# Kernel tuning notes

Hardware: AMD Instinct MI355X
Metric: run time of the kernel (lower is better)

The kernel has to match this reference:

```python
import jax, jax.numpy as jnp
import numpy as np

N, F, H, R, DEG, K = 8192, 64, 128, 3, 32, 32
TEMP = 0.3          # config.edge_temperature
NEG_SLOPE = 0.2     # LeakyReLU slope
EPS_LN = 1e-5
W_THRESH = 1e-6


def setup_inputs() -> dict:
    key = jax.random.key(0)
    ks = jax.random.split(key, 16)
    E = N * DEG
    # each node has DEG outgoing edges so no softmax row is empty (-inf everywhere)
    src = jnp.repeat(jnp.arange(N), DEG)
    tgt = jax.random.randint(ks[0], (E,), 0, N)
    edge_index = jnp.stack([src, tgt]).astype(jnp.int64)
    x = jax.random.normal(ks[1], (N, F), jnp.float32)
    edge_attr = jax.random.normal(ks[2], (E, 3), jnp.float32)
    s = lambda k, sh: jax.random.normal(k, sh, jnp.float32) * 0.05
    D = 2 * F + 3  # edge_input_dim
    params = dict(
        Ws1=s(ks[3], (D, H)), bs1=jnp.zeros(H), ln_g=jnp.ones(H), ln_b=jnp.zeros(H),
        Ws2=s(ks[4], (H, 1)), bs2=jnp.zeros(1),
        Wp=s(ks[5], (D, H)), bp=jnp.zeros(H),
        Wr1=s(ks[6], (F, H)), br1=jnp.zeros(H), Wr2=s(ks[7], (H, R)), br2=jnp.zeros(R),
        Wg1=s(ks[8], (R, H, H // 2)), bg1=jnp.zeros((R, H // 2)),
        Wg2=s(ks[9], (R, H // 2, 1)), bg2=jnp.zeros((R, 1)),
        Wc1=s(ks[10], (F, H)), bc1=jnp.zeros(H), Wc2=s(ks[11], (H, 1)), bc2=jnp.zeros(1),
    )
    return {"x": x, "edge_index": edge_index, "edge_attr": edge_attr, **params}


def reference(x, edge_index, edge_attr,
              Ws1, bs1, ln_g, ln_b, Ws2, bs2, Wp, bp,
              Wr1, br1, Wr2, br2, Wg1, bg1, Wg2, bg2,
              Wc1, bc1, Wc2, bc2):
    src, tgt = edge_index[0], edge_index[1]
    num_nodes = x.shape[0]

    # regime encoder on global mean state
    gs = x.mean(axis=0)
    regime_probs = jax.nn.softmax(jax.nn.relu(gs @ Wr1 + br1) @ Wr2 + br2)  # [R]

    # contagion detector (scalar level)
    contagion_level = jax.nn.sigmoid(jax.nn.relu(x @ Wc1 + bc1) @ Wc2 + bc2).mean()

    # gather -> edge MLP scorer with LayerNorm + LeakyReLU
    edge_input = jnp.concatenate([x[src], x[tgt], edge_attr], axis=-1)  # [E, 2F+3]
    h = edge_input @ Ws1 + bs1
    mu = h.mean(-1, keepdims=True)
    var = h.var(-1, keepdims=True)
    h = (h - mu) * jax.lax.rsqrt(var + EPS_LN) * ln_g + ln_b
    h = jnp.where(h >= 0, h, NEG_SLOPE * h)
    edge_scores_raw = h @ Ws2 + bs2  # [E, 1]

    # regime gating
    edge_hidden = jax.nn.relu(edge_input @ Wp + bp)  # [E, H]
    g1 = jax.nn.relu(jnp.einsum('eh,rhm->erm', edge_hidden, Wg1) + bg1)
    gates = jax.nn.sigmoid(jnp.einsum('erm,rmo->ero', g1, Wg2) + bg2)[..., 0]  # [E, R]
    gate_combined = (gates * regime_probs).sum(-1, keepdims=True)  # [E, 1]

    amp = 1.0 + 0.5 * contagion_level
    edge_scores = (edge_scores_raw * gate_combined * amp)[:, 0]  # [E]

    # scatter into dense NxN, masked softmax per source row, top-k
    M = jnp.full((num_nodes, num_nodes), -jnp.inf, x.dtype).at[src, tgt].set(edge_scores)
    P = jax.nn.softmax(M / TEMP, axis=-1)  # [N, N]
    topk_values, topk_indices = jax.lax.top_k(P, K)  # [N, K]

    # in-device compaction equivalent: weights below threshold zeroed (dropped edges)
    new_edge_weights = jnp.where(topk_values > W_THRESH, topk_values, 0.0)  # [N, K]
    return new_edge_weights, topk_indices
```

## Files before the change

kernel.cpp:

```cpp
#include <hip/hip_runtime.h>
#include <hip/hip_bf16.h>
#include <math.h>

#define NN 8192
#define FF 64
#define HH 128
#define RR 3
#define DEG 32
#define KK 32
#define EE (NN*DEG)
#define DD 131
#define TEMP 0.3f
#define NEG_SLOPE 0.2f
#define EPS_LN 1e-5f
#define W_THRESH 1e-6f

typedef float v2f __attribute__((ext_vector_type(2)));
__device__ __forceinline__ float4 ld4(const float* p) { return *(const float4*)p; }
#define PKFMA(a, b, c) __builtin_elementwise_fma((a), (b), (c))
#define AIDX(a, j) a[((j)>>2)*2 + (((j)&3)>>1)][(j)&1]
#define GIDX(r, g) gaccv[r][(g)>>1][(g)&1]


__global__ __launch_bounds__(256) void setup_kernel(
    const float* __restrict__ x,
    const float* __restrict__ Ws1, const float* __restrict__ Wp,
    const float* __restrict__ Wc1, const float* __restrict__ bc1,
    const float* __restrict__ Wc2, const float* __restrict__ bc2,
    float* __restrict__ PA, float* __restrict__ hdr)
{
    __shared__ float spool[12608];
    int t = threadIdx.x;
    int bid = blockIdx.x;

    if (bid < 512) {
        float* xs = spool;
        float* wl = spool + 2080;
        int which = bid & 1;
        int n0 = (bid >> 1) * 32;
        const float* base = which ? Wp : Ws1;

        for (int i = t; i < 2048; i += 256)
            xs[(i >> 6) * 65 + (i & 63)] = x[n0 * 64 + i];
        for (int it = 0; it < 8; it++) {
            int flat = (t + it * 256) * 4;
            *(float4*)&wl[flat] = ld4(&base[flat]);
        }
        __syncthreads();

        int row = t >> 3, colg = t & 7;
        float acc[16];
        #pragma unroll
        for (int j = 0; j < 16; j++) acc[j] = 0.f;
        const float* xr = &xs[row * 65];
        for (int k = 0; k < 64; k++) {
            float a = xr[k];
            const float* wr = &wl[k * 128 + colg * 16];
            #pragma unroll
            for (int jj = 0; jj < 4; jj++) {
                float4 w = ld4(wr + 4 * jj);
                acc[4*jj+0] += a * w.x; acc[4*jj+1] += a * w.y;
                acc[4*jj+2] += a * w.z; acc[4*jj+3] += a * w.w;
            }
        }
        float* outp = PA + (size_t)which * (NN * 128) + (size_t)(n0 + row) * 128 + colg * 16;
        #pragma unroll
        for (int j = 0; j < 16; j++) outp[j] = acc[j];
    } else {
        float* xs = spool;
        float* wl = spool + 4160;
        float* cs = spool + 12352;
        int n0 = (bid - 512) * 64;

        for (int i = 0; i < 16; i++) {
            int flat = t + i * 256;
            int r = flat >> 6, c = flat & 63;
            xs[r * 65 + c] = x[(n0 + r) * 64 + c];
        }
        for (int i = 0; i < 8; i++) {
            int flat = (t + i * 256) * 4;
            *(float4*)&wl[flat] = ld4(&Wc1[flat]);
        }
        __syncthreads();

        {
            int col = t & 63, g = t >> 6;
            float ps = 0.f;
            for (int r = g * 16; r < g * 16 + 16; r++) ps += xs[r * 65 + col];
            cs[g * 64 + col] = ps;
        }
        __syncthreads();
        if (t < 64) {
            float v = cs[t] + cs[64 + t] + cs[128 + t] + cs[192 + t];
            atomicAdd(&hdr[8 + t], v);
        }

        int r = t >> 2, q = t & 3;
        float accl = 0.f;
        for (int hh = 0; hh < 32; hh++) {
            int h = hh * 4 + q;
            float s = bc1[h];
            for (int i = 0; i < 64; i++) s += xs[r * 65 + i] * wl[i * 128 + h];
            accl += fmaxf(s, 0.f) * Wc2[h];
        }
        accl += __shfl_xor(accl, 1);
        accl += __shfl_xor(accl, 2);
        if (q == 0) {
            float lvl = 1.f / (1.f + expf(-(accl + bc2[0])));
            atomicAdd(&hdr[0], lvl);
        }
    }
}

__global__ __launch_bounds__(128) void regime_kernel(
    const float* __restrict__ Wr1, const float* __restrict__ br1,
    const float* __restrict__ Wr2, const float* __restrict__ br2,
    float* __restrict__ hdr)
{
    __shared__ float gsl[64];
    __shared__ float t1[128];
    int t = threadIdx.x;
    if (t < 64) gsl[t] = hdr[8 + t] * (1.f / (float)NN);
    __syncthreads();
    float a = br1[t];
    for (int i = 0; i < 64; i++) a += gsl[i] * Wr1[i * 128 + t];
    t1[t] = fmaxf(a, 0.f);
    __syncthreads();
    if (t < 3) {
        float v = br2[t];
        for (int h = 0; h < 128; h++) v += t1[h] * Wr2[h * 3 + t];
        gsl[32 + t] = v;
    }
    __syncthreads();
    if (t == 0) {
        float v0 = gsl[32], v1 = gsl[33], v2 = gsl[34];
        float m = fmaxf(v0, fmaxf(v1, v2));
        float e0 = expf(v0 - m), e1 = expf(v1 - m), e2 = expf(v2 - m);
        float inv = 1.f / (e0 + e1 + e2);
        hdr[1] = e0 * inv; hdr[2] = e1 * inv; hdr[3] = e2 * inv;
        hdr[4] = 1.f + 0.5f * (hdr[0] * (1.f / (float)NN));
    }
}

#define EIB_S 76
__global__ __launch_bounds__(256) void edge_fused_kernel(
    const int* __restrict__ tgt_idx, const float* __restrict__ edge_attr,
    const float* __restrict__ x,
    const float* __restrict__ Ws1, const float* __restrict__ bs1,
    const float* __restrict__ ln_g, const float* __restrict__ ln_b,
    const float* __restrict__ Ws2, const float* __restrict__ bs2,
    const float* __restrict__ Wp, const float* __restrict__ bp,
    const float* __restrict__ Wg1, const float* __restrict__ bg1,
    const float* __restrict__ Wg2, const float* __restrict__ bg2,
    const float* __restrict__ PA1, const float* __restrict__ PA2,
    const float* __restrict__ hdr, float* __restrict__ scores)
{
    __shared__ float pool[8000];
    float* EIB   = pool;
    float* WPan  = pool + 4864;
    float* ehTh  = pool;
    float* WgPan = pool + 4352;
    float* Gbuf  = pool;
    float* rawS  = pool + 7936;

    int t = threadIdx.x;
    int e0 = blockIdx.x * 64;

    {
        int r = t >> 2, q = t & 3;
        int ge = e0 + r;
        int tg = tgt_idx[ge];
        #pragma unroll
        for (int i = 0; i < 4; i++) {
            int col = q * 16 + 4 * i;
            *(float4*)&EIB[r * EIB_S + col] = ld4(&x[tg * 64 + col]);
        }
        if (q == 0) {
            float4 v;
            v.x = edge_attr[(size_t)ge * 3 + 0];
            v.y = edge_attr[(size_t)ge * 3 + 1];
            v.z = edge_attr[(size_t)ge * 3 + 2];
            v.w = 0.f;
            *(float4*)&EIB[r * EIB_S + 64] = v;
        } else if (q == 1) {
            *(float4*)&EIB[r * EIB_S + 68] = make_float4(0.f, 0.f, 0.f, 0.f);
        } else if (q == 2) {
            *(float4*)&EIB[r * EIB_S + 72] = make_float4(0.f, 0.f, 0.f, 0.f);
        }
    }

    int tcol = t & 7, trow = t >> 3;
    const float* EIr0 = &EIB[(2 * trow) * EIB_S];
    const float* EIr1 = EIr0 + EIB_S;
    int src = (e0 + 2 * trow) >> 5;

    v2f accs0[8], accs1[8], accp0[8], accp1[8];

    {
        const float* p1 = &PA1[(size_t)src * 128 + tcol * 4];
        const float* p2 = &PA2[(size_t)src * 128 + tcol * 4];
        #pragma unroll
        for (int jj = 0; jj < 4; jj++) {
            float4 v;
            v = ld4(p1 + jj * 32);
            v2f lo1 = { v.x, v.y }, hi1 = { v.z, v.w };
            accs0[jj*2] = lo1; accs0[jj*2+1] = hi1;
            accs1[jj*2] = lo1; accs1[jj*2+1] = hi1;
            v = ld4(p2 + jj * 32);
            v2f lo2 = { v.x, v.y }, hi2 = { v.z, v.w };
            accp0[jj*2] = lo2; accp0[jj*2+1] = hi2;
            accp1[jj*2] = lo2; accp1[jj*2+1] = hi2;
        }
    }

    for (int p = 0; p < 6; p++) {
        __syncthreads();
        #pragma unroll
        for (int i = 0; i < 3; i++) {
            int fid = i * 256 + t;
            int mat = (fid >= 384) ? 1 : 0;
            int loc = fid - mat * 384;
            int pr = loc >> 5;
            int pc = (loc & 31) * 4;
            int wrow = 64 + p * 12 + pr;
            const float* Wsrc = mat ? Wp : Ws1;
            float4 w = (wrow < 131) ? ld4(&Wsrc[wrow * 128 + pc])
                                    : make_float4(0.f, 0.f, 0.f, 0.f);
            *(float4*)&WPan[mat * 1536 + pr * 128 + pc] = w;
        }
        __syncthreads();
        for (int kk = 0; kk < 12; kk++) {
            int k = p * 12 + kk;
            float a0 = EIr0[k];
            float a1 = EIr1[k];
            v2f a0v = { a0, a0 }, a1v = { a1, a1 };
            const float* ws = &WPan[kk * 128 + tcol * 4];
            const float* wq = ws + 1536;
            #pragma unroll
            for (int jj = 0; jj < 4; jj++) {
                float4 w1 = ld4(ws + jj * 32);
                v2f w1a = { w1.x, w1.y }, w1b = { w1.z, w1.w };
                accs0[jj*2]   = PKFMA(a0v, w1a, accs0[jj*2]);
                accs0[jj*2+1] = PKFMA(a0v, w1b, accs0[jj*2+1]);
                accs1[jj*2]   = PKFMA(a1v, w1a, accs1[jj*2]);
                accs1[jj*2+1] = PKFMA(a1v, w1b, accs1[jj*2+1]);
                float4 w2 = ld4(wq + jj * 32);
                v2f w2a = { w2.x, w2.y }, w2b = { w2.z, w2.w };
                accp0[jj*2]   = PKFMA(a0v, w2a, accp0[jj*2]);
                accp0[jj*2+1] = PKFMA(a0v, w2b, accp0[jj*2+1]);
                accp1[jj*2]   = PKFMA(a1v, w2a, accp1[jj*2]);
                accp1[jj*2+1] = PKFMA(a1v, w2b, accp1[jj*2+1]);
            }
        }
    }

    {
        float s0 = 0.f, ss0 = 0.f, s1 = 0.f, ss1 = 0.f;
        #pragma unroll
        for (int j = 0; j < 16; j++) {
            int col = tcol * 4 + (j >> 2) * 32 + (j & 3);
            float b = bs1[col];
            float u0 = AIDX(accs0, j) + b;  AIDX(accs0, j) = u0;
            float u1 = AIDX(accs1, j) + b;  AIDX(accs1, j) = u1;
            s0 += u0; ss0 += u0 * u0;
            s1 += u1; ss1 += u1 * u1;
        }
        #pragma unroll
        for (int m = 1; m < 8; m <<= 1) {
            s0 += __shfl_xor(s0, m);  ss0 += __shfl_xor(ss0, m);
            s1 += __shfl_xor(s1, m);  ss1 += __shfl_xor(ss1, m);
        }
        float mu0 = s0 * (1.f / 128.f), mu1 = s1 * (1.f / 128.f);
        float var0 = ss0 * (1.f / 128.f) - mu0 * mu0;
        float var1 = ss1 * (1.f / 128.f) - mu1 * mu1;
        float inv0 = 1.f / sqrtf(var0 + EPS_LN);
        float inv1 = 1.f / sqrtf(var1 + EPS_LN);
        float d0 = 0.f, d1 = 0.f;
        #pragma unroll
        for (int j = 0; j < 16; j++) {
            int col = tcol * 4 + (j >> 2) * 32 + (j & 3);
            float g = ln_g[col], bb = ln_b[col], w2 = Ws2[col];
            float y0 = (AIDX(accs0, j) - mu0) * inv0 * g + bb;
            float y1 = (AIDX(accs1, j) - mu1) * inv1 * g + bb;
            y0 = (y0 >= 0.f) ? y0 : NEG_SLOPE * y0;
            y1 = (y1 >= 0.f) ? y1 : NEG_SLOPE * y1;
            d0 += y0 * w2; d1 += y1 * w2;
        }
        #pragma unroll
        for (int m = 1; m < 8; m <<= 1) {
            d0 += __shfl_xor(d0, m); d1 += __shfl_xor(d1, m);
        }
        if (tcol == 0) {
            rawS[2 * trow]     = d0 + bs2[0];
            rawS[2 * trow + 1] = d1 + bs2[0];
        }
    }

    int gtr = t >> 4, gtc = t & 15;
    int grow = t >> 2, gq = t & 3;

    v2f gaccv[3][8];
    #pragma unroll
    for (int rr = 0; rr < 3; rr++)
        #pragma unroll
        for (int j = 0; j < 8; j++) gaccv[rr][j] = (v2f){ 0.f, 0.f };

    for (int hf = 0; hf < 2; hf++) {
        __syncthreads();
        #pragma unroll
        for (int j2 = 0; j2 < 8; j2++) {
            int j = hf * 8 + j2;
            int col = tcol * 4 + (j >> 2) * 32 + (j & 3);
            int lc = col - hf * 64;
            float b = bp[col];
            ehTh[lc * 68 + 2 * trow]     = fmaxf(AIDX(accp0, j) + b, 0.f);
            ehTh[lc * 68 + 2 * trow + 1] = fmaxf(AIDX(accp1, j) + b, 0.f);
        }
        for (int p = 0; p < 4; p++) {
            __syncthreads();
            #pragma unroll
            for (int i = 0; i < 3; i++) {
                int fid = i * 256 + t;
                int rr = fid >> 8;
                int loc = fid & 255;
                int pr = loc >> 4;
                int pc = (loc & 15) * 4;
                *(float4*)&WgPan[rr * 1024 + pr * 64 + pc] =
                    ld4(&Wg1[(size_t)(rr * 128 + hf * 64 + p * 16 + pr) * 64 + pc]);
            }
            __syncthreads();
            for (int kk = 0; kk < 16; kk++) {
                float4 av = ld4(&ehTh[(p * 16 + kk) * 68 + 4 * gtr]);
                v2f ax = { av.x, av.x }, ay = { av.y, av.y };
                v2f az = { av.z, av.z }, aw = { av.w, av.w };
                #pragma unroll
                for (int rr = 0; rr < 3; rr++) {
                    float4 bv = ld4(&WgPan[rr * 1024 + kk * 64 + 4 * gtc]);
                    v2f bva = { bv.x, bv.y }, bvb = { bv.z, bv.w };
                    gaccv[rr][0] = PKFMA(ax, bva, gaccv[rr][0]);
                    gaccv[rr][1] = PKFMA(ax, bvb, gaccv[rr][1]);
                    gaccv[rr][2] = PKFMA(ay, bva, gaccv[rr][2]);
                    gaccv[rr][3] = PKFMA(ay, bvb, gaccv[rr][3]);
                    gaccv[rr][4] = PKFMA(az, bva, gaccv[rr][4]);
                    gaccv[rr][5] = PKFMA(az, bvb, gaccv[rr][5]);
                    gaccv[rr][6] = PKFMA(aw, bva, gaccv[rr][6]);
                    gaccv[rr][7] = PKFMA(aw, bvb, gaccv[rr][7]);
                }
            }
        }
    }

    float gc = 0.f;
    for (int rr = 0; rr < 3; rr++) {
        __syncthreads();
        #pragma unroll
        for (int j = 0; j < 4; j++) {
            float b = bg1[rr * 64 + 4 * gtc + j];
            float4 g;
            g.x = fmaxf(GIDX(rr, 0  + j) + b, 0.f);
            g.y = fmaxf(GIDX(rr, 4  + j) + b, 0.f);
            g.z = fmaxf(GIDX(rr, 8  + j) + b, 0.f);
            g.w = fmaxf(GIDX(rr, 12 + j) + b, 0.f);
            *(float4*)&Gbuf[(4 * gtc + j) * 68 + 4 * gtr] = g;
        }
        __syncthreads();
        float pacc = 0.f;
        #pragma unroll
        for (int j = 0; j < 16; j++) {
            int m = gq * 4 + (j >> 2) * 16 + (j & 3);
            pacc += Gbuf[m * 68 + grow] * Wg2[rr * 64 + m];
        }
        pacc += __shfl_xor(pacc, 1);
        pacc += __shfl_xor(pacc, 2);
        float gate = 1.f / (1.f + expf(-(pacc + bg2[rr])));
        gc += gate * hdr[1 + rr];
    }
    if (gq == 0) scores[e0 + grow] = rawS[grow] * gc * hdr[4];
}

__global__ __launch_bounds__(64) void finalize_kernel(
    const int* __restrict__ tgt_idx, const float* __restrict__ scores,
    float* __restrict__ out_w, float* __restrict__ out_i)
{
    __shared__ int   tl[32];
    __shared__ float pl[32];
    int j = threadIdx.x;
    int row = blockIdx.x;
    bool lane_active = (j < 32);
    int   tg = 0;
    float s  = -INFINITY;
    if (lane_active) {
        tg = tgt_idx[row * 32 + j];
        s  = scores[row * 32 + j];
        tl[j] = tg;
    }
    __syncthreads();

    bool alive = false;
    if (lane_active) {
        alive = true;
        for (int j2 = j + 1; j2 < 32; j2++)
            if (tl[j2] == tg) { alive = false; break; }
    }
    float z = (lane_active && alive) ? s * (1.f / TEMP) : -INFINITY;
    float m = z;
    #pragma unroll
    for (int mm = 1; mm < 64; mm <<= 1) m = fmaxf(m, __shfl_xor(m, mm));
    float p = (lane_active && alive) ? expf(z - m) : 0.f;
    float sum = p;
    #pragma unroll
    for (int mm = 1; mm < 64; mm <<= 1) sum += __shfl_xor(sum, mm);
    p = p / sum;
    if (lane_active) pl[j] = alive ? p : -1.f;
    __syncthreads();

    int rank = 0, dcount = 0;
    for (int j2 = 0; j2 < 32; j2++) {
        float pj = pl[j2];
        if (pj >= 0.f) {
            dcount++;
            if (lane_active && alive) {
                if (pj > p || (pj == p && tl[j2] < tg)) rank++;
            }
        }
    }
    if (lane_active && alive) {
        out_w[row * 32 + rank] = (p > W_THRESH) ? p : 0.f;
        out_i[row * 32 + rank] = (float)tg;
    }
    if (j == 0) {
        int c = 0;
        for (int slot = dcount; slot < 32; slot++) {
            for (;;) {
                bool found = false;
                for (int q = 0; q < 32; q++) if (tl[q] == c) { found = true; break; }
                if (!found) break;
                c++;
            }
            out_w[row * 32 + slot] = 0.f;
            out_i[row * 32 + slot] = (float)c;
            c++;
        }
    }
}

extern "C" void kernel_launch(void* const* d_in, const int* in_sizes, int n_in,
                              void* d_out, int out_size, void* d_ws, size_t ws_size,
                              hipStream_t stream)
{
    const float* x          = (const float*)d_in[0];
    const int*   edge_index = (const int*)  d_in[1];
    const float* edge_attr  = (const float*)d_in[2];
    const float* Ws1 = (const float*)d_in[3];
    const float* bs1 = (const float*)d_in[4];
    const float* ln_g = (const float*)d_in[5];
    const float* ln_b = (const float*)d_in[6];
    const float* Ws2 = (const float*)d_in[7];
    const float* bs2 = (const float*)d_in[8];
    const float* Wp  = (const float*)d_in[9];
    const float* bp  = (const float*)d_in[10];
    const float* Wr1 = (const float*)d_in[11];
    const float* br1 = (const float*)d_in[12];
    const float* Wr2 = (const float*)d_in[13];
    const float* br2 = (const float*)d_in[14];
    const float* Wg1 = (const float*)d_in[15];
    const float* bg1 = (const float*)d_in[16];
    const float* Wg2 = (const float*)d_in[17];
    const float* bg2 = (const float*)d_in[18];
    const float* Wc1 = (const float*)d_in[19];
    const float* bc1 = (const float*)d_in[20];
    const float* Wc2 = (const float*)d_in[21];
    const float* bc2 = (const float*)d_in[22];

    float* hdr    = (float*)d_ws;
    float* scores = hdr + 128;
    float* tabs   = scores + EE;
    const int* tgt = edge_index + EE;

    hipMemsetAsync(d_ws, 0, 512, stream);
    setup_kernel<<<640, 256, 0, stream>>>(x, Ws1, Wp, Wc1, bc1, Wc2, bc2, tabs, hdr);
    regime_kernel<<<1, 128, 0, stream>>>(Wr1, br1, Wr2, br2, hdr);
    edge_fused_kernel<<<EE / 64, 256, 0, stream>>>(
        tgt, edge_attr, x, Ws1, bs1, ln_g, ln_b, Ws2, bs2, Wp, bp,
        Wg1, bg1, Wg2, bg2, tabs, tabs + (size_t)NN * 128, hdr, scores);
    finalize_kernel<<<NN, 64, 0, stream>>>(
        tgt, scores, (float*)d_out, (float*)d_out + NN * KK);
}
```

Baseline: 444.6 us.

## Read edge-MLP and gate weights directly from global memory instead of LDS panels

Removes the LDS weight panels and their staging loops in the edge fused kernel, so Ws1/Wp and Wg1 rows are read straight from global memory (cached in L1/L2) inside the FMA loops. This eliminates many __syncthreads barriers and the panel copy traffic, and shrinks shared memory from 8000 to 4416 floats, allowing more resident blocks per CU. The cost is per-thread global loads in the inner loop, which may add latency that is harder to hide than LDS reads. The padding-column zeroing is dropped because the K loop now stops exactly at 67.

```diff
diff --git a/kernel.cpp b/kernel.cpp
--- a/kernel.cpp
+++ b/kernel.cpp
@@ -142,7 +142,7 @@
     }
 }
 
-#define EIB_S 76
+#define EIB_S 68
 __global__ __launch_bounds__(256) void edge_fused_kernel(
     const int* __restrict__ tgt_idx, const float* __restrict__ edge_attr,
     const float* __restrict__ x,
@@ -155,13 +155,11 @@
     const float* __restrict__ PA1, const float* __restrict__ PA2,
     const float* __restrict__ hdr, float* __restrict__ scores)
 {
-    __shared__ float pool[8000];
+    __shared__ float pool[4416];
     float* EIB   = pool;
-    float* WPan  = pool + 4864;
     float* ehTh  = pool;
-    float* WgPan = pool + 4352;
     float* Gbuf  = pool;
-    float* rawS  = pool + 7936;
+    float* rawS  = pool + 4352;
 
     int t = threadIdx.x;
     int e0 = blockIdx.x * 64;
@@ -182,10 +180,6 @@
             v.z = edge_attr[(size_t)ge * 3 + 2];
             v.w = 0.f;
             *(float4*)&EIB[r * EIB_S + 64] = v;
-        } else if (q == 1) {
-            *(float4*)&EIB[r * EIB_S + 68] = make_float4(0.f, 0.f, 0.f, 0.f);
-        } else if (q == 2) {
-            *(float4*)&EIB[r * EIB_S + 72] = make_float4(0.f, 0.f, 0.f, 0.f);
         }
     }
 
@@ -213,29 +207,18 @@
         }
     }
 
-    for (int p = 0; p < 6; p++) {
-        __syncthreads();
-        #pragma unroll
-        for (int i = 0; i < 3; i++) {
-            int fid = i * 256 + t;
-            int mat = (fid >= 384) ? 1 : 0;
-            int loc = fid - mat * 384;
-            int pr = loc >> 5;
-            int pc = (loc & 31) * 4;
-            int wrow = 64 + p * 12 + pr;
-            const float* Wsrc = mat ? Wp : Ws1;
-            float4 w = (wrow < 131) ? ld4(&Wsrc[wrow * 128 + pc])
-                                    : make_float4(0.f, 0.f, 0.f, 0.f);
-            *(float4*)&WPan[mat * 1536 + pr * 128 + pc] = w;
-        }
-        __syncthreads();
-        for (int kk = 0; kk < 12; kk++) {
-            int k = p * 12 + kk;
+    __syncthreads();
+
+    {
+        const float* wS = Ws1 + (size_t)64 * 128 + tcol * 4;
+        const float* wQ = Wp  + (size_t)64 * 128 + tcol * 4;
+        #pragma unroll 2
+        for (int k = 0; k < 64; k++) {
             float a0 = EIr0[k];
             float a1 = EIr1[k];
             v2f a0v = { a0, a0 }, a1v = { a1, a1 };
-            const float* ws = &WPan[kk * 128 + tcol * 4];
-            const float* wq = ws + 1536;
+            const float* ws = wS + (size_t)k * 128;
+            const float* wq = wQ + (size_t)k * 128;
             #pragma unroll
             for (int jj = 0; jj < 4; jj++) {
                 float4 w1 = ld4(ws + jj * 32);
@@ -252,6 +235,29 @@
                 accp1[jj*2+1] = PKFMA(a1v, w2b, accp1[jj*2+1]);
             }
         }
+        #pragma unroll
+        for (int i = 0; i < 3; i++) {
+            float a0 = EIr0[64 + i];
+            float a1 = EIr1[64 + i];
+            v2f a0v = { a0, a0 }, a1v = { a1, a1 };
+            const float* ws = Ws1 + (size_t)(128 + i) * 128 + tcol * 4;
+            const float* wq = Wp  + (size_t)(128 + i) * 128 + tcol * 4;
+            #pragma unroll
+            for (int jj = 0; jj < 4; jj++) {
+                float4 w1 = ld4(ws + jj * 32);
+                v2f w1a = { w1.x, w1.y }, w1b = { w1.z, w1.w };
+                accs0[jj*2]   = PKFMA(a0v, w1a, accs0[jj*2]);
+                accs0[jj*2+1] = PKFMA(a0v, w1b, accs0[jj*2+1]);
+                accs1[jj*2]   = PKFMA(a1v, w1a, accs1[jj*2]);
+                accs1[jj*2+1] = PKFMA(a1v, w1b, accs1[jj*2+1]);
+                float4 w2 = ld4(wq + jj * 32);
+                v2f w2a = { w2.x, w2.y }, w2b = { w2.z, w2.w };
+                accp0[jj*2]   = PKFMA(a0v, w2a, accp0[jj*2]);
+                accp0[jj*2+1] = PKFMA(a0v, w2b, accp0[jj*2+1]);
+                accp1[jj*2]   = PKFMA(a1v, w2a, accp1[jj*2]);
+                accp1[jj*2+1] = PKFMA(a1v, w2b, accp1[jj*2+1]);
+            }
+        }
     }
 
     {
@@ -305,6 +311,8 @@
         #pragma unroll
         for (int j = 0; j < 8; j++) gaccv[rr][j] = (v2f){ 0.f, 0.f };
 
+    const float* wG = Wg1 + 4 * gtc;
+
     for (int hf = 0; hf < 2; hf++) {
         __syncthreads();
         #pragma unroll
@@ -313,39 +321,28 @@
             int col = tcol * 4 + (j >> 2) * 32 + (j & 3);
             int lc = col - hf * 64;
             float b = bp[col];
-            ehTh[lc * 68 + 2 * trow]     = fmaxf(AIDX(accp0, j) + b, 0.f);
-            ehTh[lc * 68 + 2 * trow + 1] = fmaxf(AIDX(accp1, j) + b, 0.f);
-        }
-        for (int p = 0; p < 4; p++) {
-            __syncthreads();
+            ehTh[lc * EIB_S + 2 * trow]     = fmaxf(AIDX(accp0, j) + b, 0.f);
+            ehTh[lc * EIB_S + 2 * trow + 1] = fmaxf(AIDX(accp1, j) + b, 0.f);
+        }
+        __syncthreads();
+        #pragma unroll 2
+        for (int kk2 = 0; kk2 < 64; kk2++) {
+            float4 av = ld4(&ehTh[kk2 * EIB_S + 4 * gtr]);
+            v2f ax = { av.x, av.x }, ay = { av.y, av.y };
+            v2f az = { av.z, av.z }, aw = { av.w, av.w };
+            const float* wrow = wG + (size_t)(hf * 64 + kk2) * 64;
             #pragma unroll
-            for (int i = 0; i < 3; i++) {
-                int fid = i * 256 + t;
-                int rr = fid >> 8;
-                int loc = fid & 255;
-                int pr = loc >> 4;
-                int pc = (loc & 15) * 4;
-                *(float4*)&WgPan[rr * 1024 + pr * 64 + pc] =
-                    ld4(&Wg1[(size_t)(rr * 128 + hf * 64 + p * 16 + pr) * 64 + pc]);
-            }
-            __syncthreads();
-            for (int kk = 0; kk < 16; kk++) {
-                float4 av = ld4(&ehTh[(p * 16 + kk) * 68 + 4 * gtr]);
-                v2f ax = { av.x, av.x }, ay = { av.y, av.y };
-                v2f az = { av.z, av.z }, aw = { av.w, av.w };
-                #pragma unroll
-                for (int rr = 0; rr < 3; rr++) {
-                    float4 bv = ld4(&WgPan[rr * 1024 + kk * 64 + 4 * gtc]);
-                    v2f bva = { bv.x, bv.y }, bvb = { bv.z, bv.w };
-                    gaccv[rr][0] = PKFMA(ax, bva, gaccv[rr][0]);
-                    gaccv[rr][1] = PKFMA(ax, bvb, gaccv[rr][1]);
-                    gaccv[rr][2] = PKFMA(ay, bva, gaccv[rr][2]);
-                    gaccv[rr][3] = PKFMA(ay, bvb, gaccv[rr][3]);
-                    gaccv[rr][4] = PKFMA(az, bva, gaccv[rr][4]);
-                    gaccv[rr][5] = PKFMA(az, bvb, gaccv[rr][5]);
-                    gaccv[rr][6] = PKFMA(aw, bva, gaccv[rr][6]);
-                    gaccv[rr][7] = PKFMA(aw, bvb, gaccv[rr][7]);
-                }
+            for (int rr = 0; rr < 3; rr++) {
+                float4 bv = ld4(wrow + (size_t)rr * 8192);
+                v2f bva = { bv.x, bv.y }, bvb = { bv.z, bv.w };
+                gaccv[rr][0] = PKFMA(ax, bva, gaccv[rr][0]);
+                gaccv[rr][1] = PKFMA(ax, bvb, gaccv[rr][1]);
+                gaccv[rr][2] = PKFMA(ay, bva, gaccv[rr][2]);
+                gaccv[rr][3] = PKFMA(ay, bvb, gaccv[rr][3]);
+                gaccv[rr][4] = PKFMA(az, bva, gaccv[rr][4]);
+                gaccv[rr][5] = PKFMA(az, bvb, gaccv[rr][5]);
+                gaccv[rr][6] = PKFMA(aw, bva, gaccv[rr][6]);
+                gaccv[rr][7] = PKFMA(aw, bvb, gaccv[rr][7]);
             }
         }
     }
@@ -361,14 +358,14 @@
             g.y = fmaxf(GIDX(rr, 4  + j) + b, 0.f);
             g.z = fmaxf(GIDX(rr, 8  + j) + b, 0.f);
             g.w = fmaxf(GIDX(rr, 12 + j) + b, 0.f);
-            *(float4*)&Gbuf[(4 * gtc + j) * 68 + 4 * gtr] = g;
+            *(float4*)&Gbuf[(4 * gtc + j) * EIB_S + 4 * gtr] = g;
         }
         __syncthreads();
         float pacc = 0.f;
         #pragma unroll
         for (int j = 0; j < 16; j++) {
             int m = gq * 4 + (j >> 2) * 16 + (j & 3);
-            pacc += Gbuf[m * 68 + grow] * Wg2[rr * 64 + m];
+            pacc += Gbuf[m * EIB_S + grow] * Wg2[rr * 64 + m];
         }
         pacc += __shfl_xor(pacc, 1);
         pacc += __shfl_xor(pacc, 2);
```

After: 594.3 us. 1.34x slower.
